# Kernel tuning notes

Measured on AMD Instinct MI355X. Metric: run time of the kernel, lower is better.

The kernel has to match this reference:

```python
import jax, jax.numpy as jnp
import numpy as np

B, H, W, C, K, CLASSES = 16, 128, 128, 256, 32, 21
BN_EPS = 1e-3  # keras BatchNormalization default epsilon


def setup_inputs() -> dict:
    key = jax.random.key(0)
    ks = jax.random.split(key, 8)
    sup = 1.0 / np.sqrt(K * C)  # codeword init support from build()
    return {
        "inputs": jax.random.normal(ks[0], (B, H, W, C), jnp.float32),
        "codewords": jax.random.uniform(ks[1], (K, C), jnp.float32, -sup, sup),
        "smoothing": jax.random.uniform(ks[2], (K,), jnp.float32, -1.0, 0.0),
        "bn_gamma": jnp.ones((K,), jnp.float32),
        "bn_beta": jnp.zeros((K,), jnp.float32),
        "bn_mean": 0.1 * jax.random.normal(ks[3], (K,), jnp.float32),
        "bn_var": jax.random.uniform(ks[4], (K,), jnp.float32, 0.5, 1.5),
        "W_enc": jax.random.normal(ks[5], (C, C), jnp.float32) / np.sqrt(C),
        "b_enc": jnp.zeros((C,), jnp.float32),
        "W_se": jax.random.normal(ks[6], (C, CLASSES), jnp.float32) / np.sqrt(C),
        "b_se": jnp.zeros((CLASSES,), jnp.float32),
    }


def reference(inputs, codewords, smoothing, bn_gamma, bn_beta, bn_mean, bn_var,
              W_enc, b_enc, W_se, b_se):
    b, h, w, c = inputs.shape
    x = inputs.reshape(b, h * w, c)  # (B, N, C)
    # scaled-L2 squared distances ||x_n - c_k||^2 without the (B,N,K,C) residual tensor
    x2 = jnp.sum(x * x, axis=-1, keepdims=True)            # (B, N, 1)
    c2 = jnp.sum(codewords * codewords, axis=-1)           # (K,)
    d = x2 - 2.0 * jnp.einsum('bnc,kc->bnk', x, codewords) + c2  # (B, N, K)
    wgt = jax.nn.softmax(d * smoothing, axis=-1)           # (B, N, K)
    # sum_n w_nk (x_n - c_k) = (w^T x) - (sum_n w_nk) c_k
    agg = jnp.einsum('bnk,bnc->bkc', wgt, x) - jnp.sum(wgt, axis=1)[..., None] * codewords  # (B, K, C)
    # BatchNormalization(axis=-2): per-codeword params, inference mode
    bn = (agg - bn_mean[None, :, None]) * jax.lax.rsqrt(bn_var + BN_EPS)[None, :, None]
    bn = bn * bn_gamma[None, :, None] + bn_beta[None, :, None]
    enc = jnp.sum(jax.nn.relu(bn), axis=1)                 # (B, C)
    attn = jax.nn.sigmoid(enc @ W_enc + b_enc)             # (B, C)
    featuremaps_out = attn[:, None, None, :] * inputs       # (B, H, W, C)
    se_out = jax.nn.sigmoid(enc @ W_se + b_se)             # (B, classes)
    return featuremaps_out, se_out
```

## Files before the change

kernel.cpp:

```cpp
#include <hip/hip_runtime.h>
#include <hip/hip_bf16.h>
#include <math.h>

#define Bb 16
#define Hh 128
#define Ww 128
#define Cc 256
#define Kk 32
#define CLASSES 21
#define Nn (Hh*Ww)
#define TILE 256
#define TILES_PER_BATCH (Nn/TILE)
#define BLOCKS_PER_BATCH 32
#define TILES_PER_BLOCK (TILES_PER_BATCH/BLOCKS_PER_BATCH)
#define BN_EPS 1e-3f

#define WS_AGG  0
#define WS_WSUM (Bb*Kk*Cc)
#define WS_ATTN (WS_WSUM + Bb*Kk)
#define WS_TOTAL (WS_ATTN + Bb*Cc)

__global__ __launch_bounds__(256, 2) void k_encode(
    const float* __restrict__ x, const float* __restrict__ cw,
    const float* __restrict__ smo, float* __restrict__ agg,
    float* __restrict__ wsum)
{
    __shared__ float w_lds[Kk][TILE];
    __shared__ float sA[Kk], sB[Kk], sC[Kk];

    const int tid = threadIdx.x;
    const int b   = blockIdx.x / BLOCKS_PER_BATCH;
    const int sub = blockIdx.x % BLOCKS_PER_BATCH;

    if (tid < Kk) {
        float c2 = 0.f;
        const float* row = cw + tid * Cc;
        for (int j = 0; j < Cc; j += 4) {
            float4 v = *(const float4*)(row + j);
            c2 += v.x*v.x + v.y*v.y + v.z*v.z + v.w*v.w;
        }
        float s = smo[tid];
        sA[tid] = s;
        sB[tid] = -2.f * s;
        sC[tid] = c2 * s;
    }

    float acc[Kk];
    float wsacc[Kk];
#pragma unroll
    for (int k = 0; k < Kk; ++k) { acc[k] = 0.f; wsacc[k] = 0.f; }

    __syncthreads();

    const float4* cw4 = (const float4*)cw;

    for (int tt = 0; tt < TILES_PER_BLOCK; ++tt) {
        const int tile = sub + tt * BLOCKS_PER_BATCH;
        const int n0   = tile * TILE;

        const float4* xrow = (const float4*)(x + ((size_t)b * Nn + n0 + tid) * Cc);
        float d[Kk];
#pragma unroll
        for (int k = 0; k < Kk; ++k) d[k] = 0.f;
        float x2 = 0.f;

        for (int j = 0; j < Cc/4; ++j) {
            float4 xv = xrow[j];
            x2 = fmaf(xv.x, xv.x, fmaf(xv.y, xv.y, fmaf(xv.z, xv.z, fmaf(xv.w, xv.w, x2))));
#pragma unroll
            for (int k = 0; k < Kk; ++k) {
                float4 cv = cw4[k * (Cc/4) + j];
                d[k] = fmaf(xv.x, cv.x, fmaf(xv.y, cv.y, fmaf(xv.z, cv.z, fmaf(xv.w, cv.w, d[k]))));
            }
        }

        float m = -1e30f;
#pragma unroll
        for (int k = 0; k < Kk; ++k) {
            d[k] = fmaf(x2, sA[k], fmaf(d[k], sB[k], sC[k]));
            m = fmaxf(m, d[k]);
        }
        float sum = 0.f;
#pragma unroll
        for (int k = 0; k < Kk; ++k) { d[k] = __expf(d[k] - m); sum += d[k]; }
        float inv = 1.f / sum;
#pragma unroll
        for (int k = 0; k < Kk; ++k) w_lds[k][tid] = d[k] * inv;

        __syncthreads();

        const int c = tid;
        const float* xin = x + ((size_t)b * Nn + n0) * Cc + c;
        for (int n4 = 0; n4 < TILE/4; ++n4) {
            float x0 = xin[(n4*4 + 0) * Cc];
            float x1 = xin[(n4*4 + 1) * Cc];
            float x2v = xin[(n4*4 + 2) * Cc];
            float x3 = xin[(n4*4 + 3) * Cc];
#pragma unroll
            for (int k = 0; k < Kk; ++k) {
                float4 wv = *(const float4*)&w_lds[k][n4*4];
                acc[k] = fmaf(wv.x, x0, fmaf(wv.y, x1, fmaf(wv.z, x2v, fmaf(wv.w, x3, acc[k]))));
            }
        }

        if (tid < 64) {
#pragma unroll
            for (int k = 0; k < Kk; ++k) {
                float4 wv = *(const float4*)&w_lds[k][tid*4];
                float s = wv.x + wv.y + wv.z + wv.w;
#pragma unroll
                for (int off = 32; off; off >>= 1) s += __shfl_xor(s, off, 64);
                wsacc[k] += s;
            }
        }
        __syncthreads();
    }

    float* aggb = agg + (size_t)b * Kk * Cc;
#pragma unroll
    for (int k = 0; k < Kk; ++k) atomicAdd(aggb + k * Cc + tid, acc[k]);
    if (tid == 0) {
#pragma unroll
        for (int k = 0; k < Kk; ++k) atomicAdd(wsum + b * Kk + k, wsacc[k]);
    }
}

__global__ __launch_bounds__(256) void k_head(
    const float* __restrict__ agg, const float* __restrict__ wsum,
    const float* __restrict__ cw,
    const float* __restrict__ gamma, const float* __restrict__ beta,
    const float* __restrict__ mean, const float* __restrict__ var,
    const float* __restrict__ W_enc, const float* __restrict__ b_enc,
    const float* __restrict__ W_se, const float* __restrict__ b_se,
    float* __restrict__ attn, float* __restrict__ se_out)
{
    __shared__ float enc[Cc];
    const int b = blockIdx.x, c = threadIdx.x;

    float e = 0.f;
#pragma unroll
    for (int k = 0; k < Kk; ++k) {
        float a = agg[((size_t)b * Kk + k) * Cc + c] - wsum[b * Kk + k] * cw[k * Cc + c];
        float bnv = (a - mean[k]) * (1.0f / sqrtf(var[k] + BN_EPS)) * gamma[k] + beta[k];
        e += fmaxf(bnv, 0.f);
    }
    enc[c] = e;
    __syncthreads();

    float s = b_enc[c];
    for (int j = 0; j < Cc; ++j) s = fmaf(enc[j], W_enc[j * Cc + c], s);
    attn[b * Cc + c] = 1.f / (1.f + __expf(-s));

    if (c < CLASSES) {
        float q = b_se[c];
        for (int j = 0; j < Cc; ++j) q = fmaf(enc[j], W_se[j * CLASSES + c], q);
        se_out[b * CLASSES + c] = 1.f / (1.f + __expf(-q));
    }
}

__global__ __launch_bounds__(256) void k_scale(
    const float4* __restrict__ xin, const float* __restrict__ attn,
    float4* __restrict__ out)
{
    const int total = Bb * Nn * Cc / 4;
    int i = blockIdx.x * 256 + threadIdx.x;
    const int stride = gridDim.x * 256;
    for (; i < total; i += stride) {
        int b  = i >> 20;
        int c4 = i & (Cc/4 - 1);
        float4 a = *(const float4*)(attn + b * Cc + c4 * 4);
        float4 v = xin[i];
        v.x *= a.x; v.y *= a.y; v.z *= a.z; v.w *= a.w;
        out[i] = v;
    }
}

extern "C" void kernel_launch(void* const* d_in, const int* in_sizes, int n_in,
                              void* d_out, int out_size, void* d_ws, size_t ws_size,
                              hipStream_t stream)
{
    const float* x     = (const float*)d_in[0];
    const float* cw    = (const float*)d_in[1];
    const float* smo   = (const float*)d_in[2];
    const float* gamma = (const float*)d_in[3];
    const float* beta  = (const float*)d_in[4];
    const float* mean  = (const float*)d_in[5];
    const float* var   = (const float*)d_in[6];
    const float* W_enc = (const float*)d_in[7];
    const float* b_enc = (const float*)d_in[8];
    const float* W_se  = (const float*)d_in[9];
    const float* b_se  = (const float*)d_in[10];

    float* ws   = (float*)d_ws;
    float* agg  = ws + WS_AGG;
    float* wsum = ws + WS_WSUM;
    float* attn = ws + WS_ATTN;

    float* fm_out = (float*)d_out;
    float* se_out = fm_out + (size_t)Bb * Nn * Cc;

    hipMemsetAsync(d_ws, 0, WS_TOTAL * sizeof(float), stream);

    k_encode<<<Bb * BLOCKS_PER_BATCH, 256, 0, stream>>>(x, cw, smo, agg, wsum);
    k_head<<<Bb, Cc, 0, stream>>>(agg, wsum, cw, gamma, beta, mean, var,
                                  W_enc, b_enc, W_se, b_se, attn, se_out);
    k_scale<<<2048, 256, 0, stream>>>((const float4*)x, attn, (float4*)d_out);
}
```

Before: 779.9 us.

## Restructure encode kernel with LDS-staged register-tiled distance and aggregation

Rewrites the encode kernel to handle one 256-pixel tile per block (1024 blocks instead of 512). The distance GEMM now stages x chunks (with a skewed transposed layout) and codeword slices in LDS, and each thread computes a 4-pixel by 8-codeword register tile. The aggregation step is split so each wave handles a 16-codeword by 128-pixel slab with 4x16 accumulators. Per-thread global reads of whole pixel rows and the uncoalesced codeword loads are replaced by cooperative coalesced loads, aiming to raise arithmetic intensity and occupancy. The cost is more global atomics per block and more LDS traffic and synchronisation.

```diff
diff --git a/kernel.cpp b/kernel.cpp
--- a/kernel.cpp
+++ b/kernel.cpp
@@ -10,9 +10,6 @@
 #define CLASSES 21
 #define Nn (Hh*Ww)
 #define TILE 256
-#define TILES_PER_BATCH (Nn/TILE)
-#define BLOCKS_PER_BATCH 32
-#define TILES_PER_BLOCK (TILES_PER_BATCH/BLOCKS_PER_BATCH)
 #define BN_EPS 1e-3f
 
 #define WS_AGG  0
@@ -20,109 +17,164 @@
 #define WS_ATTN (WS_WSUM + Bb*Kk)
 #define WS_TOTAL (WS_ATTN + Bb*Cc)
 
-__global__ __launch_bounds__(256, 2) void k_encode(
+__global__ __launch_bounds__(256, 4) void k_encode(
     const float* __restrict__ x, const float* __restrict__ cw,
     const float* __restrict__ smo, float* __restrict__ agg,
     float* __restrict__ wsum)
 {
-    __shared__ float w_lds[Kk][TILE];
+    __shared__ float xs[32 * 256];
+    __shared__ float cs[32][32];
     __shared__ float sA[Kk], sB[Kk], sC[Kk];
-
-    const int tid = threadIdx.x;
-    const int b   = blockIdx.x / BLOCKS_PER_BATCH;
-    const int sub = blockIdx.x % BLOCKS_PER_BATCH;
+    __shared__ float wsumS[Kk];
+
+    const int tid  = threadIdx.x;
+    const int lane = tid & 63;
+    const int wv   = tid >> 6;
+    const int b    = blockIdx.x >> 6;
+    const int tile = blockIdx.x & 63;
+    const int n0   = tile * TILE;
+    const float* xb = x + ((size_t)b * Nn + n0) * Cc;
 
     if (tid < Kk) {
         float c2 = 0.f;
-        const float* row = cw + tid * Cc;
-        for (int j = 0; j < Cc; j += 4) {
-            float4 v = *(const float4*)(row + j);
+        const float4* row = (const float4*)(cw + tid * Cc);
+        for (int j = 0; j < Cc/4; ++j) {
+            float4 v = row[j];
             c2 += v.x*v.x + v.y*v.y + v.z*v.z + v.w*v.w;
         }
         float s = smo[tid];
-        sA[tid] = s;
-        sB[tid] = -2.f * s;
-        sC[tid] = c2 * s;
-    }
-
-    float acc[Kk];
-    float wsacc[Kk];
-#pragma unroll
-    for (int k = 0; k < Kk; ++k) { acc[k] = 0.f; wsacc[k] = 0.f; }
-
-    __syncthreads();
-
-    const float4* cw4 = (const float4*)cw;
-
-    for (int tt = 0; tt < TILES_PER_BLOCK; ++tt) {
-        const int tile = sub + tt * BLOCKS_PER_BATCH;
-        const int n0   = tile * TILE;
-
-        const float4* xrow = (const float4*)(x + ((size_t)b * Nn + n0 + tid) * Cc);
-        float d[Kk];
-#pragma unroll
-        for (int k = 0; k < Kk; ++k) d[k] = 0.f;
-        float x2 = 0.f;
-
-        for (int j = 0; j < Cc/4; ++j) {
-            float4 xv = xrow[j];
-            x2 = fmaf(xv.x, xv.x, fmaf(xv.y, xv.y, fmaf(xv.z, xv.z, fmaf(xv.w, xv.w, x2))));
-#pragma unroll
-            for (int k = 0; k < Kk; ++k) {
-                float4 cv = cw4[k * (Cc/4) + j];
-                d[k] = fmaf(xv.x, cv.x, fmaf(xv.y, cv.y, fmaf(xv.z, cv.z, fmaf(xv.w, cv.w, d[k]))));
+        sA[tid] = s; sB[tid] = -2.f * s; sC[tid] = c2 * s;
+        wsumS[tid] = 0.f;
+    }
+
+    const int px0 = (tid & 63) * 4;
+    const int k0  = (tid >> 6) * 8;
+    float4 d4[8];
+    float4 x2v = make_float4(0.f, 0.f, 0.f, 0.f);
+#pragma unroll
+    for (int j = 0; j < 8; ++j) d4[j] = make_float4(0.f, 0.f, 0.f, 0.f);
+
+    for (int ch = 0; ch < 8; ++ch) {
+        const int c0 = ch * 32;
+        __syncthreads();
+        {
+            int k  = tid & 31;
+            int cb = (tid >> 5) << 2;
+            const float* src = cw + k * Cc + c0 + cb;
+            cs[cb+0][k] = src[0];
+            cs[cb+1][k] = src[1];
+            cs[cb+2][k] = src[2];
+            cs[cb+3][k] = src[3];
+        }
+#pragma unroll
+        for (int i = 0; i < 8; ++i) {
+            int f  = tid + (i << 8);
+            int p  = f >> 3;
+            int c4 = f & 7;
+            float4 v = *(const float4*)(xb + (size_t)p * Cc + c0 + (c4 << 2));
+            int q = (p + (c4 << 2)) & 255;
+            xs[(4*c4 + 0) * 256 + q] = v.x;
+            xs[(4*c4 + 1) * 256 + q] = v.y;
+            xs[(4*c4 + 2) * 256 + q] = v.z;
+            xs[(4*c4 + 3) * 256 + q] = v.w;
+        }
+        __syncthreads();
+#pragma unroll
+        for (int c = 0; c < 32; ++c) {
+            int q = (px0 + ((c >> 2) << 2)) & 255;
+            float4 xv = *(const float4*)&xs[c * 256 + q];
+            x2v.x = fmaf(xv.x, xv.x, x2v.x);
+            x2v.y = fmaf(xv.y, xv.y, x2v.y);
+            x2v.z = fmaf(xv.z, xv.z, x2v.z);
+            x2v.w = fmaf(xv.w, xv.w, x2v.w);
+            float4 ck0 = *(const float4*)&cs[c][k0];
+            float4 ck1 = *(const float4*)&cs[c][k0 + 4];
+            const float ck[8] = {ck0.x, ck0.y, ck0.z, ck0.w, ck1.x, ck1.y, ck1.z, ck1.w};
+#pragma unroll
+            for (int j = 0; j < 8; ++j) {
+                d4[j].x = fmaf(xv.x, ck[j], d4[j].x);
+                d4[j].y = fmaf(xv.y, ck[j], d4[j].y);
+                d4[j].z = fmaf(xv.z, ck[j], d4[j].z);
+                d4[j].w = fmaf(xv.w, ck[j], d4[j].w);
             }
         }
-
-        float m = -1e30f;
+    }
+
+    __syncthreads();
+    float* warr = xs;
+#pragma unroll
+    for (int j = 0; j < 8; ++j) {
+        int k = k0 + j;
+        float4 a;
+        a.x = fmaf(x2v.x, sA[k], fmaf(d4[j].x, sB[k], sC[k]));
+        a.y = fmaf(x2v.y, sA[k], fmaf(d4[j].y, sB[k], sC[k]));
+        a.z = fmaf(x2v.z, sA[k], fmaf(d4[j].z, sB[k], sC[k]));
+        a.w = fmaf(x2v.w, sA[k], fmaf(d4[j].w, sB[k], sC[k]));
+        *(float4*)&warr[k * 256 + px0] = a;
+    }
+    __syncthreads();
+
+    {
+        float v[Kk];
+        float m = -3.4e38f;
+#pragma unroll
+        for (int k = 0; k < Kk; ++k) { v[k] = warr[k * 256 + tid]; m = fmaxf(m, v[k]); }
+        float sum = 0.f;
+#pragma unroll
+        for (int k = 0; k < Kk; ++k) { v[k] = __expf(v[k] - m); sum += v[k]; }
+        float inv = 1.f / sum;
 #pragma unroll
         for (int k = 0; k < Kk; ++k) {
-            d[k] = fmaf(x2, sA[k], fmaf(d[k], sB[k], sC[k]));
-            m = fmaxf(m, d[k]);
-        }
-        float sum = 0.f;
-#pragma unroll
-        for (int k = 0; k < Kk; ++k) { d[k] = __expf(d[k] - m); sum += d[k]; }
-        float inv = 1.f / sum;
-#pragma unroll
-        for (int k = 0; k < Kk; ++k) w_lds[k][tid] = d[k] * inv;
-
-        __syncthreads();
-
-        const int c = tid;
-        const float* xin = x + ((size_t)b * Nn + n0) * Cc + c;
-        for (int n4 = 0; n4 < TILE/4; ++n4) {
-            float x0 = xin[(n4*4 + 0) * Cc];
-            float x1 = xin[(n4*4 + 1) * Cc];
-            float x2v = xin[(n4*4 + 2) * Cc];
-            float x3 = xin[(n4*4 + 3) * Cc];
-#pragma unroll
-            for (int k = 0; k < Kk; ++k) {
-                float4 wv = *(const float4*)&w_lds[k][n4*4];
-                acc[k] = fmaf(wv.x, x0, fmaf(wv.y, x1, fmaf(wv.z, x2v, fmaf(wv.w, x3, acc[k]))));
+            float wk = v[k] * inv;
+            warr[k * 256 + tid] = wk;
+            float r = wk;
+#pragma unroll
+            for (int off = 32; off; off >>= 1) r += __shfl_xor(r, off, 64);
+            if (lane == 0) atomicAdd(&wsumS[k], r);
+        }
+    }
+    __syncthreads();
+    if (tid < Kk) atomicAdd(wsum + b * Kk + tid, wsumS[tid]);
+
+    const int kh = wv & 1;
+    const int nh = wv >> 1;
+    const int kb = kh * 16;
+    float acc[4][16];
+#pragma unroll
+    for (int j = 0; j < 4; ++j)
+#pragma unroll
+        for (int kk = 0; kk < 16; ++kk) acc[j][kk] = 0.f;
+
+    for (int n4 = 0; n4 < 32; ++n4) {
+        const int n = nh * 128 + n4 * 4;
+        float xr[4][4];
+#pragma unroll
+        for (int i = 0; i < 4; ++i) {
+            const float* xrow = xb + (size_t)(n + i) * Cc + lane;
+            xr[i][0] = xrow[0];
+            xr[i][1] = xrow[64];
+            xr[i][2] = xrow[128];
+            xr[i][3] = xrow[192];
+        }
+#pragma unroll
+        for (int kk = 0; kk < 16; ++kk) {
+            float4 wv4 = *(const float4*)&warr[(kb + kk) * 256 + n];
+#pragma unroll
+            for (int j = 0; j < 4; ++j) {
+                acc[j][kk] = fmaf(wv4.x, xr[0][j],
+                             fmaf(wv4.y, xr[1][j],
+                             fmaf(wv4.z, xr[2][j],
+                             fmaf(wv4.w, xr[3][j], acc[j][kk]))));
             }
         }
-
-        if (tid < 64) {
-#pragma unroll
-            for (int k = 0; k < Kk; ++k) {
-                float4 wv = *(const float4*)&w_lds[k][tid*4];
-                float s = wv.x + wv.y + wv.z + wv.w;
-#pragma unroll
-                for (int off = 32; off; off >>= 1) s += __shfl_xor(s, off, 64);
-                wsacc[k] += s;
-            }
-        }
-        __syncthreads();
-    }
-
-    float* aggb = agg + (size_t)b * Kk * Cc;
-#pragma unroll
-    for (int k = 0; k < Kk; ++k) atomicAdd(aggb + k * Cc + tid, acc[k]);
-    if (tid == 0) {
-#pragma unroll
-        for (int k = 0; k < Kk; ++k) atomicAdd(wsum + b * Kk + k, wsacc[k]);
-    }
+    }
+
+    float* aggb = agg + ((size_t)b * Kk + kb) * Cc;
+#pragma unroll
+    for (int kk = 0; kk < 16; ++kk)
+#pragma unroll
+        for (int j = 0; j < 4; ++j)
+            atomicAdd(aggb + kk * Cc + lane + 64 * j, acc[j][kk]);
 }
 
 __global__ __launch_bounds__(256) void k_head(
@@ -201,7 +253,7 @@
 
     hipMemsetAsync(d_ws, 0, WS_TOTAL * sizeof(float), stream);
 
-    k_encode<<<Bb * BLOCKS_PER_BATCH, 256, 0, stream>>>(x, cw, smo, agg, wsum);
+    k_encode<<<Bb * 64, 256, 0, stream>>>(x, cw, smo, agg, wsum);
     k_head<<<Bb, Cc, 0, stream>>>(agg, wsum, cw, gamma, beta, mean, var,
                                   W_enc, b_enc, W_se, b_se, attn, se_out);
     k_scale<<<2048, 256, 0, stream>>>((const float4*)x, attn, (float4*)d_out);
```

Result: faster. 633.6 us (-18.8%).
